# Optimization experiments

Hardware: AMD Instinct MI355X
Metric: run time of the kernel (lower is better)

Reference implementation:

```python
import jax, jax.numpy as jnp
import numpy as np

B, S, DIM = 2, 2048, 2048
INTER = 1024          # moe_inter_dim
E = 8                 # n_routed_experts
K = 2                 # n_activated_experts
N_SHARED = 1
ROUTE_SCALE = 1.0


def setup_inputs() -> dict:
    key = jax.random.key(0)
    ks = jax.random.split(key, 8)
    s_in = 1.0 / np.sqrt(DIM)
    s_hid = 1.0 / np.sqrt(INTER)
    return {
        "x": jax.random.normal(ks[0], (B, S, DIM), dtype=jnp.float32),
        "gate_w": jax.random.normal(ks[1], (E, DIM), dtype=jnp.float32) * s_in,
        "w1": jax.random.normal(ks[2], (E, INTER, DIM), dtype=jnp.float32) * s_in,
        "w2": jax.random.normal(ks[3], (E, DIM, INTER), dtype=jnp.float32) * s_hid,
        "w3": jax.random.normal(ks[4], (E, INTER, DIM), dtype=jnp.float32) * s_in,
        "ws1": jax.random.normal(ks[5], (N_SHARED * INTER, DIM), dtype=jnp.float32) * s_in,
        "ws2": jax.random.normal(ks[6], (DIM, N_SHARED * INTER), dtype=jnp.float32) * s_hid,
        "ws3": jax.random.normal(ks[7], (N_SHARED * INTER, DIM), dtype=jnp.float32) * s_in,
    }


def reference(x, gate_w, w1, w2, w3, ws1, ws2, ws3):
    shape = x.shape
    xf = x.reshape(-1, DIM)                         # [T, d]
    # --- Gate: softmax scores, top-k (single group => plain top-k) ---
    scores = jax.nn.softmax(xf @ gate_w.T, axis=-1)  # [T, E]
    weights, idx = jax.lax.top_k(scores, K)          # [T, K]
    weights = weights * ROUTE_SCALE
    # --- Routed experts (dense compute + one-hot combine) ---
    h = jnp.einsum('td,eid->eti', xf, w1)            # [E, T, inter]
    g = jax.nn.silu(h) * jnp.einsum('td,eid->eti', xf, w3)
    eo = jnp.einsum('eti,edi->etd', g, w2)           # [E, T, d]
    comb = jnp.einsum('tke,tk->te', jax.nn.one_hot(idx, E, dtype=xf.dtype), weights)
    y = jnp.einsum('etd,te->td', eo, comb)           # [T, d]
    # --- Shared expert MLP (SwiGLU) ---
    z = (jax.nn.silu(xf @ ws1.T) * (xf @ ws3.T)) @ ws2.T
    return (y + z).reshape(shape)
```

## Files before the change

kernel.cpp:

```cpp
#include <hip/hip_runtime.h>
#include <stdint.h>

#define T_TOK 4096
#define DIM   2048
#define INTER 1024
#define NE    9
#define NPAIR 12288

typedef float v4f __attribute__((ext_vector_type(4)));
typedef short v8s __attribute__((ext_vector_type(8)));

__device__ __forceinline__ unsigned short f2bf(float f) {
    unsigned u = __float_as_uint(f);
    u += 0x7fffu + ((u >> 16) & 1u);
    return (unsigned short)(u >> 16);
}

__device__ __forceinline__ void gload_lds16(const void* g, void* l) {
    __builtin_amdgcn_global_load_lds(
        (const __attribute__((address_space(1))) void*)g,
        (__attribute__((address_space(3))) void*)l, 16, 0, 0);
}

__global__ __launch_bounds__(256) void cvt_w13_kernel(
        const float* __restrict__ w1,  const float* __restrict__ ws1, unsigned short* __restrict__ w1b,
        const float* __restrict__ w3,  const float* __restrict__ ws3, unsigned short* __restrict__ w3b,
        int* __restrict__ meta) {
    if (blockIdx.x == 0 && blockIdx.y == 0 && threadIdx.x < 18) meta[threadIdx.x] = 0;
    int which = blockIdx.y;
    const float* wmain = (which == 0) ? w1  : w3;
    const float* wsh   = (which == 0) ? ws1 : ws3;
    unsigned short* dst = (which == 0) ? w1b : w3b;
    long long i = (long long)blockIdx.x * 256 + threadIdx.x;
    long long base = i * 4;
    int e = (int)(base >> 21);
    long long within = base & ((1ll << 21) - 1);
    const float* src = (e < 8) ? (wmain + ((long long)e << 21) + within) : (wsh + within);
    float4 f = *(const float4*)src;
    ushort4 u;
    u.x = f2bf(f.x); u.y = f2bf(f.y); u.z = f2bf(f.z); u.w = f2bf(f.w);
    *(ushort4*)(dst + base) = u;
}

__global__ __launch_bounds__(256) void gate_kernel(const float* __restrict__ x,
                                                   const float* __restrict__ gw,
                                                   float* __restrict__ wt,
                                                   int* __restrict__ ei,
                                                   unsigned short* __restrict__ xb) {
    __shared__ float xs[DIM];
    __shared__ float lg[8];
    int t = blockIdx.x;
    const float* xrow = x + (size_t)t * DIM;
    for (int i = threadIdx.x; i < DIM / 4; i += 256)
        ((float4*)xs)[i] = ((const float4*)xrow)[i];
    __syncthreads();
    for (int i = threadIdx.x; i < DIM / 4; i += 256) {
        float4 f = ((const float4*)xs)[i];
        ushort4 u;
        u.x = f2bf(f.x); u.y = f2bf(f.y); u.z = f2bf(f.z); u.w = f2bf(f.w);
        ((ushort4*)(xb + (size_t)t * DIM))[i] = u;
    }
    int e = threadIdx.x >> 5;
    int l = threadIdx.x & 31;
    const float* g = gw + (size_t)e * DIM;
    float p = 0.f;
    #pragma unroll 8
    for (int d = l; d < DIM; d += 32) p += xs[d] * g[d];
    for (int m = 16; m >= 1; m >>= 1) p += __shfl_xor(p, m, 32);
    if (l == 0) lg[e] = p;
    __syncthreads();
    if (threadIdx.x == 0) {
        float mx = lg[0];
        for (int i = 1; i < 8; i++) mx = fmaxf(mx, lg[i]);
        float pr[8], s = 0.f;
        for (int i = 0; i < 8; i++) { pr[i] = __expf(lg[i] - mx); s += pr[i]; }
        float inv = 1.f / s;
        float b1 = -1.f, b2 = -1.f; int i1 = 0, i2 = 0;
        for (int i = 0; i < 8; i++) {
            float v = pr[i] * inv;
            if (v > b1)      { b2 = b1; i2 = i1; b1 = v; i1 = i; }
            else if (v > b2) { b2 = v;  i2 = i; }
        }
        wt[t * 3 + 0] = b1; wt[t * 3 + 1] = b2; wt[t * 3 + 2] = 1.f;
        ei[t * 3 + 0] = i1; ei[t * 3 + 1] = i2; ei[t * 3 + 2] = 8;
    }
}

__global__ __launch_bounds__(256) void count_kernel(const int* __restrict__ ei,
                                                    int* __restrict__ meta) {
    __shared__ int lcnt[NE];
    if (threadIdx.x < NE) lcnt[threadIdx.x] = 0;
    __syncthreads();
    int t = blockIdx.x * 256 + threadIdx.x;
    #pragma unroll
    for (int s = 0; s < 3; s++) atomicAdd(&lcnt[ei[t * 3 + s]], 1);
    __syncthreads();
    if (threadIdx.x < NE) atomicAdd(&meta[threadIdx.x], lcnt[threadIdx.x]);
}

__global__ __launch_bounds__(256) void fill_kernel(const int* __restrict__ ei,
                                                   const float* __restrict__ wt,
                                                   int* __restrict__ meta,
                                                   int* __restrict__ pair_tok,
                                                   float* __restrict__ pair_w,
                                                   int* __restrict__ slots) {
    __shared__ int lcnt[NE], lbase[NE], loffs[NE];
    if (threadIdx.x < NE) lcnt[threadIdx.x] = 0;
    __syncthreads();
    int t = blockIdx.x * 256 + threadIdx.x;
    int es[3], lp[3];
    #pragma unroll
    for (int s = 0; s < 3; s++) {
        es[s] = ei[t * 3 + s];
        lp[s] = atomicAdd(&lcnt[es[s]], 1);
    }
    __syncthreads();
    if (threadIdx.x < NE)
        lbase[threadIdx.x] = atomicAdd(&meta[9 + threadIdx.x], lcnt[threadIdx.x]);
    if (threadIdx.x == 0) {
        int a = 0;
        #pragma unroll
        for (int e = 0; e < NE; e++) { loffs[e] = a; a += meta[e]; }
    }
    __syncthreads();
    #pragma unroll
    for (int s = 0; s < 3; s++) {
        int g = loffs[es[s]] + lbase[es[s]] + lp[s];
        pair_tok[g] = t;
        pair_w[g] = wt[t * 3 + s];
        slots[t * 3 + s] = g;
    }
}

__global__ __launch_bounds__(256, 3) void gemm1_kernel(
        const unsigned short* __restrict__ xb,
        const unsigned short* __restrict__ w1b,
        const unsigned short* __restrict__ w3b,
        unsigned short* __restrict__ G,
        const int* __restrict__ meta,
        const int* __restrict__ pair_tok,
        const float* __restrict__ pair_w,
        const float* __restrict__ w2f,
        const float* __restrict__ ws2,
        unsigned short* __restrict__ w2b) {
    if (blockIdx.y >= 32) {
        int flat = (blockIdx.z * 8 + (blockIdx.y - 32)) * 16 + blockIdx.x;
        long long vbase = (long long)flat * 4096 + threadIdx.x;
        #pragma unroll
        for (int it = 0; it < 16; ++it) {
            long long i = vbase + it * 256;
            long long base = i * 4;
            int e = (int)(base >> 21);
            long long within = base & ((1ll << 21) - 1);
            const float* src = (e < 8) ? (w2f + ((long long)e << 21) + within) : (ws2 + within);
            float4 f = *(const float4*)src;
            ushort4 u;
            u.x = f2bf(f.x); u.y = f2bf(f.y); u.z = f2bf(f.z); u.w = f2bf(f.w);
            *(ushort4*)(w2b + base) = u;
        }
        return;
    }
    int e = blockIdx.z;
    int cnt = meta[e];
    int m0 = blockIdx.y * 128;
    if (m0 >= cnt) return;
    int off = 0;
    for (int i = 0; i < e; i++) off += meta[i];
    int n0 = blockIdx.x * 64;

    __shared__ __align__(16) unsigned short As[128 * 64];
    __shared__ __align__(16) unsigned short B1s[64 * 64];
    __shared__ __align__(16) unsigned short B3s[64 * 64];

    int tid = threadIdx.x;
    int wave = tid >> 6, lane = tid & 63;
    int kc = (lane & 7) ^ (lane >> 3);

    const unsigned short* sbase;
    unsigned short* ldst;
    unsigned soff[8];
    if (wave < 2) {
        sbase = xb;
        ldst = As + wave * 4096;
        #pragma unroll
        for (int j = 0; j < 8; j++) {
            int row = (wave * 8 + j) * 8 + (lane >> 3);
            int p = m0 + row; p = p < cnt ? p : cnt - 1;
            int tok = pair_tok[off + p];
            soff[j] = (unsigned)tok * DIM + (unsigned)(kc * 8);
        }
    } else {
        const unsigned short* wsrc = (wave == 2) ? w1b : w3b;
        ldst = (wave == 2) ? B1s : B3s;
        sbase = wsrc + ((size_t)e * INTER + n0 + (lane >> 3)) * DIM + kc * 8;
    }

    int wm = wave >> 1, wn = wave & 1;
    int mb = wm * 64, nb = wn * 32;
    v4f zero4 = {0.f, 0.f, 0.f, 0.f};
    v4f acc1[4][2], acc3[4][2];
    #pragma unroll
    for (int i = 0; i < 4; i++)
        #pragma unroll
        for (int j = 0; j < 2; j++) { acc1[i][j] = zero4; acc3[i][j] = zero4; }

    for (int k0 = 0; k0 < DIM; k0 += 64) {
        if (wave < 2) {
            #pragma unroll
            for (int j = 0; j < 8; j++)
                gload_lds16(sbase + soff[j] + k0, ldst + j * 512);
        } else {
            #pragma unroll
            for (int j = 0; j < 8; j++)
                gload_lds16(sbase + (unsigned)(j * 8 * DIM) + k0, ldst + j * 512);
        }
        __syncthreads();
        #pragma unroll
        for (int s = 0; s < 2; s++) {
            int kk = s * 4 + (lane >> 4);
            v8s a[4], b1[2], b3[2];
            #pragma unroll
            for (int mt = 0; mt < 4; mt++) {
                int r = mb + mt * 16 + (lane & 15);
                a[mt] = *(const v8s*)&As[r * 64 + ((kk ^ (r & 7)) << 3)];
            }
            #pragma unroll
            for (int nt = 0; nt < 2; nt++) {
                int n = nb + nt * 16 + (lane & 15);
                int o = n * 64 + ((kk ^ (n & 7)) << 3);
                b1[nt] = *(const v8s*)&B1s[o];
                b3[nt] = *(const v8s*)&B3s[o];
            }
            #pragma unroll
            for (int mt = 0; mt < 4; mt++)
                #pragma unroll
                for (int nt = 0; nt < 2; nt++) {
                    acc1[mt][nt] = __builtin_amdgcn_mfma_f32_16x16x32_bf16(a[mt], b1[nt], acc1[mt][nt], 0, 0, 0);
                    acc3[mt][nt] = __builtin_amdgcn_mfma_f32_16x16x32_bf16(a[mt], b3[nt], acc3[mt][nt], 0, 0, 0);
                }
        }
        __syncthreads();
    }

    #pragma unroll
    for (int mt = 0; mt < 4; mt++) {
        #pragma unroll
        for (int r = 0; r < 4; r++) {
            int row = mb + mt * 16 + ((lane >> 4) << 2) + r;
            int p = m0 + row;
            if (p < cnt) {
                float w = pair_w[off + p];
                size_t gbase = (size_t)(off + p) * INTER + n0 + nb;
                #pragma unroll
                for (int nt = 0; nt < 2; nt++) {
                    float h1 = acc1[mt][nt][r];
                    float h3 = acc3[mt][nt][r];
                    float gv = h1 / (1.f + __expf(-h1)) * h3 * w;
                    G[gbase + nt * 16 + (lane & 15)] = f2bf(gv);
                }
            }
        }
    }
}

__global__ __launch_bounds__(256, 3) void gemm2_kernel(
        const unsigned short* __restrict__ G,
        const unsigned short* __restrict__ w2b,
        unsigned short* __restrict__ eo,
        const int* __restrict__ meta) {
    int e = blockIdx.z;
    int cnt = meta[e];
    int m0 = blockIdx.y * 128;
    if (m0 >= cnt) return;
    int off = 0;
    for (int i = 0; i < e; i++) off += meta[i];
    int n0 = blockIdx.x * 128;

    __shared__ __align__(16) unsigned short As[128 * 64];
    __shared__ __align__(16) unsigned short Bs[128 * 64];

    int tid = threadIdx.x;
    int wave = tid >> 6, lane = tid & 63;
    int kc = (lane & 7) ^ (lane >> 3);

    const unsigned short* sbase;
    unsigned short* ldst;
    unsigned soff[8];
    if (wave < 2) {
        sbase = G;
        ldst = As + wave * 4096;
        #pragma unroll
        for (int j = 0; j < 8; j++) {
            int row = (wave * 8 + j) * 8 + (lane >> 3);
            int p = m0 + row; p = p < cnt ? p : cnt - 1;
            soff[j] = (unsigned)(off + p) * INTER + (unsigned)(kc * 8);
        }
    } else {
        int g0 = (wave - 2) * 64;
        ldst = Bs + (wave - 2) * 4096;
        sbase = w2b + ((size_t)e * DIM + n0 + g0 + (lane >> 3)) * INTER + kc * 8;
    }

    int wm = wave >> 1, wn = wave & 1;
    int mb = wm * 64, nbw = wn * 64;
    v4f zero4 = {0.f, 0.f, 0.f, 0.f};
    v4f acc[4][4];
    #pragma unroll
    for (int i = 0; i < 4; i++)
        #pragma unroll
        for (int j = 0; j < 4; j++) acc[i][j] = zero4;

    for (int k0 = 0; k0 < INTER; k0 += 64) {
        if (wave < 2) {
            #pragma unroll
            for (int j = 0; j < 8; j++)
                gload_lds16(sbase + soff[j] + k0, ldst + j * 512);
        } else {
            #pragma unroll
            for (int j = 0; j < 8; j++)
                gload_lds16(sbase + (unsigned)(j * 8 * INTER) + k0, ldst + j * 512);
        }
        __syncthreads();
        #pragma unroll
        for (int s = 0; s < 2; s++) {
            int kk = s * 4 + (lane >> 4);
            v8s a[4], b[4];
            #pragma unroll
            for (int mt = 0; mt < 4; mt++) {
                int r = mb + mt * 16 + (lane & 15);
                a[mt] = *(const v8s*)&As[r * 64 + ((kk ^ (r & 7)) << 3)];
            }
            #pragma unroll
            for (int nt = 0; nt < 4; nt++) {
                int n = nbw + nt * 16 + (lane & 15);
                b[nt] = *(const v8s*)&Bs[n * 64 + ((kk ^ (n & 7)) << 3)];
            }
            #pragma unroll
            for (int mt = 0; mt < 4; mt++)
                #pragma unroll
                for (int nt = 0; nt < 4; nt++)
                    acc[mt][nt] = __builtin_amdgcn_mfma_f32_16x16x32_bf16(a[mt], b[nt], acc[mt][nt], 0, 0, 0);
        }
        __syncthreads();
    }

    #pragma unroll
    for (int mt = 0; mt < 4; mt++) {
        #pragma unroll
        for (int r = 0; r < 4; r++) {
            int row = mb + mt * 16 + ((lane >> 4) << 2) + r;
            int p = m0 + row;
            if (p < cnt) {
                unsigned short* obase = eo + (size_t)(off + p) * DIM + n0 + nbw;
                #pragma unroll
                for (int nt = 0; nt < 4; nt++)
                    obase[nt * 16 + (lane & 15)] = f2bf(acc[mt][nt][r]);
            }
        }
    }
}

__global__ __launch_bounds__(256) void combine_kernel(const unsigned short* __restrict__ eo,
                                                      const int* __restrict__ slots,
                                                      float* __restrict__ out) {
    int t = blockIdx.x;
    int p0 = slots[t * 3 + 0], p1 = slots[t * 3 + 1], p2 = slots[t * 3 + 2];
    const ushort4* r0 = (const ushort4*)(eo + (size_t)p0 * DIM);
    const ushort4* r1 = (const ushort4*)(eo + (size_t)p1 * DIM);
    const ushort4* r2 = (const ushort4*)(eo + (size_t)p2 * DIM);
    float4* o = (float4*)(out + (size_t)t * DIM);
    for (int i = threadIdx.x; i < DIM / 4; i += 256) {
        ushort4 a = r0[i], b = r1[i], c = r2[i];
        float4 v;
        v.x = __uint_as_float((unsigned)a.x << 16) + __uint_as_float((unsigned)b.x << 16) + __uint_as_float((unsigned)c.x << 16);
        v.y = __uint_as_float((unsigned)a.y << 16) + __uint_as_float((unsigned)b.y << 16) + __uint_as_float((unsigned)c.y << 16);
        v.z = __uint_as_float((unsigned)a.z << 16) + __uint_as_float((unsigned)b.z << 16) + __uint_as_float((unsigned)c.z << 16);
        v.w = __uint_as_float((unsigned)a.w << 16) + __uint_as_float((unsigned)b.w << 16) + __uint_as_float((unsigned)c.w << 16);
        o[i] = v;
    }
}

extern "C" void kernel_launch(void* const* d_in, const int* in_sizes, int n_in,
                              void* d_out, int out_size, void* d_ws, size_t ws_size,
                              hipStream_t stream) {
    const float* x   = (const float*)d_in[0];
    const float* gw  = (const float*)d_in[1];
    const float* w1  = (const float*)d_in[2];
    const float* w2  = (const float*)d_in[3];
    const float* w3  = (const float*)d_in[4];
    const float* ws1 = (const float*)d_in[5];
    const float* ws2 = (const float*)d_in[6];
    const float* ws3 = (const float*)d_in[7];
    float* out = (float*)d_out;

    char* p = (char*)d_ws;
    auto alloc = [&](size_t bytes) {
        void* r = (void*)p;
        p += (bytes + 255) & ~(size_t)255;
        return r;
    };
    unsigned short* xb  = (unsigned short*)alloc((size_t)T_TOK * DIM * 2);
    unsigned short* w1b = (unsigned short*)alloc((size_t)NE * INTER * DIM * 2);
    unsigned short* w3b = (unsigned short*)alloc((size_t)NE * INTER * DIM * 2);
    unsigned short* w2b = (unsigned short*)alloc((size_t)NE * DIM * INTER * 2);
    unsigned short* G   = (unsigned short*)alloc((size_t)NPAIR * INTER * 2);
    int*   ei    = (int*)alloc((size_t)T_TOK * 3 * 4);
    float* wt    = (float*)alloc((size_t)T_TOK * 3 * 4);
    int*   ptok  = (int*)alloc((size_t)NPAIR * 4);
    float* pw    = (float*)alloc((size_t)NPAIR * 4);
    int*   slots = (int*)alloc((size_t)NPAIR * 4);
    int*   meta  = (int*)alloc(32 * 4);
    unsigned short* eo = w1b;

    int wgrid = (NE * INTER * DIM / 4) / 256;
    cvt_w13_kernel<<<dim3(wgrid, 2), 256, 0, stream>>>(w1, ws1, w1b, w3, ws3, w3b, meta);
    gate_kernel<<<T_TOK, 256, 0, stream>>>(x, gw, wt, ei, xb);
    count_kernel<<<T_TOK / 256, 256, 0, stream>>>(ei, meta);
    fill_kernel<<<T_TOK / 256, 256, 0, stream>>>(ei, wt, meta, ptok, pw, slots);
    gemm1_kernel<<<dim3(INTER / 64, 40, NE), 256, 0, stream>>>(xb, w1b, w3b, G, meta, ptok, pw,
                                                               w2, ws2, w2b);
    gemm2_kernel<<<dim3(DIM / 128, 32, NE), 256, 0, stream>>>(G, w2b, eo, meta);
    combine_kernel<<<T_TOK, 256, 0, stream>>>(eo, slots, out);
}
```

Measured before the change: 445.0 us.

## Fuse weight conversion with gating kernel and swizzle GEMM block order for XCDs

Merges the w1/w3 bf16 conversion and the gate/x-conversion kernels into a single launch, using a third grid row for the per-token gating work, which removes one kernel launch and lets the two run concurrently. Both expert GEMMs now remap the flat block index with an 8-way stride swizzle, so that blocks dispatched round-robin across the 8 XCDs land on contiguous tiles of the same expert. This is meant to improve per-XCD L2 reuse of weight and activation tiles. The prep grid launches many idle blocks in its third row, since only the first T_TOK of them do gating work.

New measurement: 574.3 us. 29.1% more time.

```diff
diff --git a/kernel.cpp b/kernel.cpp
--- a/kernel.cpp
+++ b/kernel.cpp
@@ -22,34 +22,34 @@
         (__attribute__((address_space(3))) void*)l, 16, 0, 0);
 }
 
-__global__ __launch_bounds__(256) void cvt_w13_kernel(
+__global__ __launch_bounds__(256) void prep_kernel(
         const float* __restrict__ w1,  const float* __restrict__ ws1, unsigned short* __restrict__ w1b,
         const float* __restrict__ w3,  const float* __restrict__ ws3, unsigned short* __restrict__ w3b,
+        const float* __restrict__ x,   const float* __restrict__ gw,
+        float* __restrict__ wt,        int* __restrict__ ei,
+        unsigned short* __restrict__ xb,
         int* __restrict__ meta) {
-    if (blockIdx.x == 0 && blockIdx.y == 0 && threadIdx.x < 18) meta[threadIdx.x] = 0;
-    int which = blockIdx.y;
-    const float* wmain = (which == 0) ? w1  : w3;
-    const float* wsh   = (which == 0) ? ws1 : ws3;
-    unsigned short* dst = (which == 0) ? w1b : w3b;
-    long long i = (long long)blockIdx.x * 256 + threadIdx.x;
-    long long base = i * 4;
-    int e = (int)(base >> 21);
-    long long within = base & ((1ll << 21) - 1);
-    const float* src = (e < 8) ? (wmain + ((long long)e << 21) + within) : (wsh + within);
-    float4 f = *(const float4*)src;
-    ushort4 u;
-    u.x = f2bf(f.x); u.y = f2bf(f.y); u.z = f2bf(f.z); u.w = f2bf(f.w);
-    *(ushort4*)(dst + base) = u;
-}
-
-__global__ __launch_bounds__(256) void gate_kernel(const float* __restrict__ x,
-                                                   const float* __restrict__ gw,
-                                                   float* __restrict__ wt,
-                                                   int* __restrict__ ei,
-                                                   unsigned short* __restrict__ xb) {
+    if (blockIdx.y < 2) {
+        if (blockIdx.x == 0 && blockIdx.y == 0 && threadIdx.x < 18) meta[threadIdx.x] = 0;
+        int which = blockIdx.y;
+        const float* wmain = (which == 0) ? w1  : w3;
+        const float* wsh   = (which == 0) ? ws1 : ws3;
+        unsigned short* dst = (which == 0) ? w1b : w3b;
+        long long i = (long long)blockIdx.x * 256 + threadIdx.x;
+        long long base = i * 4;
+        int e = (int)(base >> 21);
+        long long within = base & ((1ll << 21) - 1);
+        const float* src = (e < 8) ? (wmain + ((long long)e << 21) + within) : (wsh + within);
+        float4 f = *(const float4*)src;
+        ushort4 u;
+        u.x = f2bf(f.x); u.y = f2bf(f.y); u.z = f2bf(f.z); u.w = f2bf(f.w);
+        *(ushort4*)(dst + base) = u;
+        return;
+    }
+    int t = blockIdx.x;
+    if (t >= T_TOK) return;
     __shared__ float xs[DIM];
     __shared__ float lg[8];
-    int t = blockIdx.x;
     const float* xrow = x + (size_t)t * DIM;
     for (int i = threadIdx.x; i < DIM / 4; i += 256)
         ((float4*)xs)[i] = ((const float4*)xrow)[i];
@@ -143,16 +143,23 @@
         const float* __restrict__ w2f,
         const float* __restrict__ ws2,
         unsigned short* __restrict__ w2b) {
-    if (blockIdx.y >= 32) {
-        int flat = (blockIdx.z * 8 + (blockIdx.y - 32)) * 16 + blockIdx.x;
+    unsigned F = (blockIdx.z * 40u + blockIdx.y) * 16u + blockIdx.x;
+    unsigned swz = (F & 7u) * 720u + (F >> 3);
+    int e = (int)(swz / 640u);
+    unsigned rem = swz - (unsigned)e * 640u;
+    int by = (int)(rem >> 4);
+    int bx = (int)(rem & 15u);
+
+    if (by >= 32) {
+        int flat = (e * 8 + (by - 32)) * 16 + bx;
         long long vbase = (long long)flat * 4096 + threadIdx.x;
         #pragma unroll
         for (int it = 0; it < 16; ++it) {
             long long i = vbase + it * 256;
             long long base = i * 4;
-            int e = (int)(base >> 21);
+            int ew = (int)(base >> 21);
             long long within = base & ((1ll << 21) - 1);
-            const float* src = (e < 8) ? (w2f + ((long long)e << 21) + within) : (ws2 + within);
+            const float* src = (ew < 8) ? (w2f + ((long long)ew << 21) + within) : (ws2 + within);
             float4 f = *(const float4*)src;
             ushort4 u;
             u.x = f2bf(f.x); u.y = f2bf(f.y); u.z = f2bf(f.z); u.w = f2bf(f.w);
@@ -160,13 +167,12 @@
         }
         return;
     }
-    int e = blockIdx.z;
     int cnt = meta[e];
-    int m0 = blockIdx.y * 128;
+    int m0 = by * 128;
     if (m0 >= cnt) return;
     int off = 0;
     for (int i = 0; i < e; i++) off += meta[i];
-    int n0 = blockIdx.x * 64;
+    int n0 = bx * 64;
 
     __shared__ __align__(16) unsigned short As[128 * 64];
     __shared__ __align__(16) unsigned short B1s[64 * 64];
@@ -268,13 +274,19 @@
         const unsigned short* __restrict__ w2b,
         unsigned short* __restrict__ eo,
         const int* __restrict__ meta) {
-    int e = blockIdx.z;
+    unsigned F = (blockIdx.z * 32u + blockIdx.y) * 16u + blockIdx.x;
+    unsigned swz = (F & 7u) * 576u + (F >> 3);
+    int e = (int)(swz / 512u);
+    unsigned rem = swz & 511u;
+    int by = (int)(rem >> 4);
+    int bx = (int)(rem & 15u);
+
     int cnt = meta[e];
-    int m0 = blockIdx.y * 128;
+    int m0 = by * 128;
     if (m0 >= cnt) return;
     int off = 0;
     for (int i = 0; i < e; i++) off += meta[i];
-    int n0 = blockIdx.x * 128;
+    int n0 = bx * 128;
 
     __shared__ __align__(16) unsigned short As[128 * 64];
     __shared__ __align__(16) unsigned short Bs[128 * 64];
@@ -413,8 +425,8 @@
     unsigned short* eo = w1b;
 
     int wgrid = (NE * INTER * DIM / 4) / 256;
-    cvt_w13_kernel<<<dim3(wgrid, 2), 256, 0, stream>>>(w1, ws1, w1b, w3, ws3, w3b, meta);
-    gate_kernel<<<T_TOK, 256, 0, stream>>>(x, gw, wt, ei, xb);
+    prep_kernel<<<dim3(wgrid, 3), 256, 0, stream>>>(w1, ws1, w1b, w3, ws3, w3b,
+                                                    x, gw, wt, ei, xb, meta);
     count_kernel<<<T_TOK / 256, 256, 0, stream>>>(ei, meta);
     fill_kernel<<<T_TOK / 256, 256, 0, stream>>>(ei, wt, meta, ptok, pw, slots);
     gemm1_kernel<<<dim3(INTER / 64, 40, NE), 256, 0, stream>>>(xb, w1b, w3b, G, meta, ptok, pw,
```
